# Optimization experiments

Hardware: AMD Instinct MI355X
Metric: run time of the kernel (lower is better)

The kernel has to match this reference:

```python
import jax, jax.numpy as jnp
import numpy as np

EMBED_DIM = 256
SEQ_LEN = 4096
BATCH = 8
ALPHA = 0.99


def setup_inputs() -> dict:
    key = jax.random.key(0)
    k_x, k_w, k_b = jax.random.split(key, 3)
    x = jax.random.normal(k_x, (BATCH, SEQ_LEN, EMBED_DIM), dtype=jnp.float32)
    # nn.Linear(embed_dim, 3*embed_dim): store as [d, 3d] so y = x @ Wqkv + bqkv
    Wqkv = jax.random.normal(k_w, (EMBED_DIM, 3 * EMBED_DIM), dtype=jnp.float32) * (EMBED_DIM ** -0.5)
    bqkv = jax.random.normal(k_b, (3 * EMBED_DIM,), dtype=jnp.float32) * 0.02
    return {"x": x, "Wqkv": Wqkv, "bqkv": bqkv}


def reference(x, Wqkv, bqkv):
    bs, sl, d = x.shape
    qkv = x @ Wqkv + bqkv                      # [bs, sl, 3d]
    q, k, v = jnp.split(qkv, 3, axis=-1)       # each [bs, sl, d]
    # causal * exponential-decay mask: M[i, j] = alpha**(i-j) for j <= i else 0
    i = jnp.arange(sl, dtype=jnp.float32)
    M = jnp.where(i[:, None] >= i[None, :],
                  jnp.power(jnp.float32(ALPHA), i[:, None] - i[None, :]),
                  0.0)                          # [sl, sl]
    scores = jnp.einsum('bqd,bkd->bqk', q, k) / jnp.sqrt(jnp.float32(d))
    out = jnp.einsum('bqk,bkd->bqd', scores * M, v)
    return out
```

## Files before the change

### kernel.cpp

```cpp
#include <hip/hip_runtime.h>

typedef __bf16 bf16x8 __attribute__((ext_vector_type(8)));
typedef float f32x4 __attribute__((ext_vector_type(4)));
typedef unsigned short u16;
typedef unsigned int u32;
typedef u16 u16x4 __attribute__((ext_vector_type(4)));
typedef u16 u16x8 __attribute__((ext_vector_type(8)));

#define L2ALPHA (-0.014499569f)
#define WIN 1024

static __device__ __forceinline__ u16 f2bf(float f) {
    u32 u = __builtin_bit_cast(u32, f);
    return (u16)((u + 0x7FFFu + ((u >> 16) & 1u)) >> 16);
}

static __device__ __forceinline__ void gl2lds16(const void* g, void* l) {
    __builtin_amdgcn_global_load_lds(
        (const __attribute__((address_space(1))) u32*)g,
        (__attribute__((address_space(3))) u32*)l, 16, 0, 0);
}

__global__ __launch_bounds__(256, 2) void proj_kernel(
        const float* __restrict__ x, const float* __restrict__ Wq,
        const float* __restrict__ bias,
        u16* __restrict__ qb, u16* __restrict__ kb, u16* __restrict__ vb)
{
    __shared__ __align__(16) u16 Bs[32 * 128 * 8];
    __shared__ __align__(16) u16 As[4][32 * 40];

    const int tid = threadIdx.x, lane = tid & 63, w = tid >> 6;
    const int l = blockIdx.x;
    const int nb = l % 6;
    const int mt = l / 6;
    const int m0 = mt * 128, n0 = nb * 128;
    const int m = lane & 15, quad = lane >> 4;

    {
        const int col = tid & 127;
        const int khalf = tid >> 7;
        #pragma unroll
        for (int s = 0; s < 32; ++s) {
            int k0 = (khalf + 2 * s) * 4;
            u16x4 h;
            #pragma unroll
            for (int i = 0; i < 4; ++i)
                h[i] = f2bf(Wq[(k0 + i) * 768 + n0 + col]);
            *(u16x4*)&Bs[((k0 >> 3) * 128 + col) * 8 + (k0 & 7)] = h;
        }
    }
    __syncthreads();

    const int r = lane & 31, h = lane >> 5;
    const float* xrow = x + (size_t)(m0 + w * 32 + r) * 256 + h * 16;
    u16* As_w = &As[w][0];

    f32x4 acc[2][8];
    #pragma unroll
    for (int rt = 0; rt < 2; ++rt)
        #pragma unroll
        for (int ct = 0; ct < 8; ++ct)
            acc[rt][ct] = f32x4{0.f, 0.f, 0.f, 0.f};

    float4 g0 = *(const float4*)(xrow + 0);
    float4 g1 = *(const float4*)(xrow + 4);
    float4 g2 = *(const float4*)(xrow + 8);
    float4 g3 = *(const float4*)(xrow + 12);

    for (int kt = 0; kt < 8; ++kt) {
        u16x8 ha, hb;
        ha[0]=f2bf(g0.x); ha[1]=f2bf(g0.y); ha[2]=f2bf(g0.z); ha[3]=f2bf(g0.w);
        ha[4]=f2bf(g1.x); ha[5]=f2bf(g1.y); ha[6]=f2bf(g1.z); ha[7]=f2bf(g1.w);
        hb[0]=f2bf(g2.x); hb[1]=f2bf(g2.y); hb[2]=f2bf(g2.z); hb[3]=f2bf(g2.w);
        hb[4]=f2bf(g3.x); hb[5]=f2bf(g3.y); hb[6]=f2bf(g3.z); hb[7]=f2bf(g3.w);
        *(u16x8*)&As_w[r * 40 + h * 16]     = ha;
        *(u16x8*)&As_w[r * 40 + h * 16 + 8] = hb;

        if (kt < 7) {
            const float* xn = xrow + (kt + 1) * 32;
            g0 = *(const float4*)(xn + 0);
            g1 = *(const float4*)(xn + 4);
            g2 = *(const float4*)(xn + 8);
            g3 = *(const float4*)(xn + 12);
        }

        asm volatile("s_waitcnt lgkmcnt(0)" ::: "memory");

        bf16x8 af[2], bfr[8];
        #pragma unroll
        for (int rt = 0; rt < 2; ++rt)
            af[rt] = *(const bf16x8*)&As_w[(rt * 16 + m) * 40 + quad * 8];
        #pragma unroll
        for (int ct = 0; ct < 8; ++ct)
            bfr[ct] = *(const bf16x8*)&Bs[((kt * 4 + quad) * 128 + ct * 16 + m) * 8];
        #pragma unroll
        for (int rt = 0; rt < 2; ++rt)
            #pragma unroll
            for (int ct = 0; ct < 8; ++ct)
                acc[rt][ct] = __builtin_amdgcn_mfma_f32_16x16x32_bf16(
                    af[rt], bfr[ct], acc[rt][ct], 0, 0, 0);
    }

    const int b = m0 >> 12;
    const int jbase = (m0 & 4095) + w * 32;
    const int d0 = (nb & 1) * 128;

    if (nb < 2) {
        #pragma unroll
        for (int rt = 0; rt < 2; ++rt)
            #pragma unroll
            for (int ct = 0; ct < 8; ++ct) {
                int coll = ct * 16 + m;
                float bv = bias[d0 + coll];
                #pragma unroll
                for (int rr = 0; rr < 4; ++rr) {
                    int row = m0 + w * 32 + rt * 16 + quad * 4 + rr;
                    qb[(size_t)row * 256 + d0 + coll] = f2bf((acc[rt][ct][rr] + bv) * 0.0625f);
                }
            }
    } else if (nb < 4) {
        #pragma unroll
        for (int rt = 0; rt < 2; ++rt)
            #pragma unroll
            for (int ct = 0; ct < 8; ++ct) {
                int d = d0 + ct * 16 + m;
                float bv = bias[256 + d];
                int k8 = d >> 5, qk = (d >> 3) & 3, e = d & 7;
                #pragma unroll
                for (int rr = 0; rr < 4; ++rr) {
                    int j = jbase + rt * 16 + quad * 4 + rr;
                    int jt = j >> 5, jj = j & 31;
                    kb[((((size_t)(b * 128 + jt) * 2 + (jj & 1)) * 8 + k8) * 64 + qk * 16 + (jj >> 1)) * 8 + e]
                        = f2bf(acc[rt][ct][rr] + bv);
                }
            }
    } else {
        #pragma unroll
        for (int rt = 0; rt < 2; ++rt)
            #pragma unroll
            for (int ct = 0; ct < 8; ++ct) {
                int d = d0 + ct * 16 + m;
                float bv = bias[512 + d];
                int dt = d >> 4, mv = d & 15;
                int j = jbase + rt * 16 + quad * 4;
                int jt = j >> 5, qv = (j >> 3) & 3, e0 = j & 7;
                u16x4 hv;
                #pragma unroll
                for (int rr = 0; rr < 4; ++rr) hv[rr] = f2bf(acc[rt][ct][rr] + bv);
                *(u16x4*)&vb[(((size_t)(b * 128 + jt) * 16 + dt) * 64 + qv * 16 + mv) * 8 + e0] = hv;
            }
    }
}

__global__ __launch_bounds__(512, 2) void attn_kernel(
        const u16* __restrict__ qb, const u16* __restrict__ kb,
        const u16* __restrict__ vb, float* __restrict__ out)
{
    __shared__ __align__(16) u16 RB[4][16384];
    __shared__ __align__(16) u16 Ps[8 * 16 * 40];

    const int tid = threadIdx.x, lane = tid & 63, w = tid >> 6;
    const int l = blockIdx.x;
    const int b = l & 7;
    const int m0 = (l >> 3) * 128;
    const int qrow0 = m0 + w * 16;
    const int m = lane & 15, quad = lane >> 4;
    const size_t rowbase = (size_t)b * 4096;
    const size_t pbase = (size_t)b * 128;

    bf16x8 qf[8];
    #pragma unroll
    for (int k8 = 0; k8 < 8; ++k8)
        qf[k8] = *(const bf16x8*)(qb + (rowbase + qrow0 + m) * 256 + k8 * 32 + quad * 8);
    asm volatile("s_waitcnt vmcnt(0)" ::: "memory");

    float Arow[4];
    #pragma unroll
    for (int rr = 0; rr < 4; ++rr)
        Arow[rr] = __builtin_amdgcn_exp2f((float)(quad * 4 + rr) * L2ALPHA);
    const float Em0 = __builtin_amdgcn_exp2f((float)(-2 * m) * L2ALPHA);
    const float Em1 = __builtin_amdgcn_exp2f((float)(-2 * m - 1) * L2ALPHA);

    f32x4 acc[16];
    #pragma unroll
    for (int dt = 0; dt < 16; ++dt)
        acc[dt] = f32x4{0.f, 0.f, 0.f, 0.f};

    int t0 = (m0 - WIN) >> 5; if (t0 < 0) t0 = 0;
    const int t1 = (m0 >> 5) + 3;
    const int nT = t1 - t0 + 1;

    #define STAGE(ix)                                                       \
        do {                                                                \
            const int buf_ = (ix) & 3;                                      \
            const u16* kp_ = kb + (pbase + t0 + (ix)) * 8192;               \
            const u16* vp_ = vb + (pbase + t0 + (ix)) * 8192;               \
            _Pragma("unroll")                                               \
            for (int s_ = 0; s_ < 2; ++s_) {                                \
                int c_ = tid + 512 * s_;                                    \
                gl2lds16(kp_ + (size_t)c_ * 8, &RB[buf_][c_ * 8]);          \
                gl2lds16(vp_ + (size_t)c_ * 8, &RB[buf_][8192 + c_ * 8]);   \
            }                                                               \
        } while (0)

    STAGE(0); STAGE(1); STAGE(2);

    for (int it = 0; it < nT; ++it) {
        if (it <= nT - 3)      asm volatile("s_waitcnt vmcnt(8)" ::: "memory");
        else if (it == nT - 2) asm volatile("s_waitcnt vmcnt(4)" ::: "memory");
        else                   asm volatile("s_waitcnt vmcnt(0)" ::: "memory");
        __builtin_amdgcn_s_barrier();
        asm volatile("" ::: "memory");

        if (it + 3 < nT) STAGE(it + 3);

        const int t = t0 + it;
        const int j0 = t * 32;
        if (j0 <= qrow0 + 15 && j0 + (WIN + 31) >= qrow0) {
            const u16* Kt = &RB[it & 3][0];
            const u16* Vt = &RB[it & 3][8192];

            const float base = __builtin_amdgcn_exp2f((float)(qrow0 - j0) * L2ALPHA);
            const float C0 = base * Em0, C1 = base * Em1;
            const bool needMask = (j0 + 31 > qrow0);

            f32x4 sA{0.f,0.f,0.f,0.f}, sB{0.f,0.f,0.f,0.f};
            #pragma unroll
            for (int k8 = 0; k8 < 8; ++k8) {
                bf16x8 bf0 = *(const bf16x8*)&Kt[(k8 * 64 + lane) * 8];
                sA = __builtin_amdgcn_mfma_f32_16x16x32_bf16(qf[k8], bf0, sA, 0, 0, 0);
            }
            #pragma unroll
            for (int k8 = 0; k8 < 8; ++k8) {
                bf16x8 bf1 = *(const bf16x8*)&Kt[((8 + k8) * 64 + lane) * 8];
                sB = __builtin_amdgcn_mfma_f32_16x16x32_bf16(qf[k8], bf1, sB, 0, 0, 0);
            }

            if (needMask) {
                #pragma unroll
                for (int rr = 0; rr < 4; ++rr) {
                    int ioff = quad * 4 + rr;
                    int dd0 = (qrow0 - j0) + ioff - 2 * m;
                    float w0 = (dd0 >= 0) ? Arow[rr] * C0 : 0.0f;
                    float w1 = (dd0 >= 1) ? Arow[rr] * C1 : 0.0f;
                    u32 pv = (u32)f2bf(sA[rr] * w0) | ((u32)f2bf(sB[rr] * w1) << 16);
                    *(u32*)&Ps[(w * 16 + ioff) * 40 + 2 * m] = pv;
                }
            } else {
                #pragma unroll
                for (int rr = 0; rr < 4; ++rr) {
                    int ioff = quad * 4 + rr;
                    float w0 = Arow[rr] * C0;
                    float w1 = Arow[rr] * C1;
                    u32 pv = (u32)f2bf(sA[rr] * w0) | ((u32)f2bf(sB[rr] * w1) << 16);
                    *(u32*)&Ps[(w * 16 + ioff) * 40 + 2 * m] = pv;
                }
            }
            asm volatile("s_waitcnt lgkmcnt(0)" ::: "memory");

            bf16x8 pa = *(const bf16x8*)&Ps[(w * 16 + m) * 40 + quad * 8];

            #pragma unroll
            for (int dt = 0; dt < 16; ++dt) {
                bf16x8 vf = *(const bf16x8*)&Vt[(dt * 64 + lane) * 8];
                acc[dt] = __builtin_amdgcn_mfma_f32_16x16x32_bf16(pa, vf, acc[dt], 0, 0, 0);
            }
        }
    }

    #pragma unroll
    for (int dt = 0; dt < 16; ++dt)
        #pragma unroll
        for (int rr = 0; rr < 4; ++rr)
            out[(rowbase + qrow0 + quad * 4 + rr) * 256 + dt * 16 + m] = acc[dt][rr];
}

extern "C" void kernel_launch(void* const* d_in, const int* in_sizes, int n_in,
                              void* d_out, int out_size, void* d_ws, size_t ws_size,
                              hipStream_t stream) {
    (void)in_sizes; (void)n_in; (void)out_size; (void)ws_size;
    const float* x    = (const float*)d_in[0];
    const float* Wq   = (const float*)d_in[1];
    const float* bias = (const float*)d_in[2];
    float* outp = (float*)d_out;

    const size_t per = (size_t)8 * 4096 * 256;
    u16* qb = (u16*)d_ws;
    u16* kb = qb + per;
    u16* vb = kb + per;

    proj_kernel<<<1536, 256, 0, stream>>>(x, Wq, bias, qb, kb, vb);
    attn_kernel<<<256, 512, 0, stream>>>(qb, kb, vb, outp);
}
```

Measured before the change: 176.6 us.

## Give each attention wave 32 query rows to reuse K/V fragments

The attention block shrinks from 8 waves to 4, and each wave now handles two 16-row query groups. Every K and V fragment read from LDS therefore feeds two MFMAs instead of one, halving LDS read traffic per FLOP. The cost is more registers per wave (two accumulator sets, two Q fragment sets), launch bounds dropping to 1 block per SIMD set, and fewer waves to hide latency. Staging loads double per thread, and the vmcnt thresholds are adjusted to match.

```diff
diff --git a/kernel.cpp b/kernel.cpp
--- a/kernel.cpp
+++ b/kernel.cpp
@@ -152,39 +152,45 @@
     }
 }
 
-__global__ __launch_bounds__(512, 2) void attn_kernel(
+__global__ __launch_bounds__(256, 1) void attn_kernel(
         const u16* __restrict__ qb, const u16* __restrict__ kb,
         const u16* __restrict__ vb, float* __restrict__ out)
 {
     __shared__ __align__(16) u16 RB[4][16384];
-    __shared__ __align__(16) u16 Ps[8 * 16 * 40];
+    __shared__ __align__(16) u16 Ps[4 * 32 * 40];
 
     const int tid = threadIdx.x, lane = tid & 63, w = tid >> 6;
     const int l = blockIdx.x;
     const int b = l & 7;
     const int m0 = (l >> 3) * 128;
-    const int qrow0 = m0 + w * 16;
+    const int qrow0 = m0 + w * 32;
     const int m = lane & 15, quad = lane >> 4;
     const size_t rowbase = (size_t)b * 4096;
     const size_t pbase = (size_t)b * 128;
 
-    bf16x8 qf[8];
-    #pragma unroll
-    for (int k8 = 0; k8 < 8; ++k8)
-        qf[k8] = *(const bf16x8*)(qb + (rowbase + qrow0 + m) * 256 + k8 * 32 + quad * 8);
+    bf16x8 qf[2][8];
+    #pragma unroll
+    for (int rg = 0; rg < 2; ++rg)
+        #pragma unroll
+        for (int k8 = 0; k8 < 8; ++k8)
+            qf[rg][k8] = *(const bf16x8*)(qb + (rowbase + qrow0 + rg * 16 + m) * 256 + k8 * 32 + quad * 8);
     asm volatile("s_waitcnt vmcnt(0)" ::: "memory");
 
-    float Arow[4];
-    #pragma unroll
-    for (int rr = 0; rr < 4; ++rr)
-        Arow[rr] = __builtin_amdgcn_exp2f((float)(quad * 4 + rr) * L2ALPHA);
+    float Arow[2][4];
+    #pragma unroll
+    for (int rg = 0; rg < 2; ++rg)
+        #pragma unroll
+        for (int rr = 0; rr < 4; ++rr)
+            Arow[rg][rr] = __builtin_amdgcn_exp2f((float)(rg * 16 + quad * 4 + rr) * L2ALPHA);
     const float Em0 = __builtin_amdgcn_exp2f((float)(-2 * m) * L2ALPHA);
     const float Em1 = __builtin_amdgcn_exp2f((float)(-2 * m - 1) * L2ALPHA);
 
-    f32x4 acc[16];
-    #pragma unroll
-    for (int dt = 0; dt < 16; ++dt)
-        acc[dt] = f32x4{0.f, 0.f, 0.f, 0.f};
+    f32x4 acc[2][16];
+    #pragma unroll
+    for (int rg = 0; rg < 2; ++rg)
+        #pragma unroll
+        for (int dt = 0; dt < 16; ++dt)
+            acc[rg][dt] = f32x4{0.f, 0.f, 0.f, 0.f};
 
     int t0 = (m0 - WIN) >> 5; if (t0 < 0) t0 = 0;
     const int t1 = (m0 >> 5) + 3;
@@ -196,8 +202,8 @@
             const u16* kp_ = kb + (pbase + t0 + (ix)) * 8192;               \
             const u16* vp_ = vb + (pbase + t0 + (ix)) * 8192;               \
             _Pragma("unroll")                                               \
-            for (int s_ = 0; s_ < 2; ++s_) {                                \
-                int c_ = tid + 512 * s_;                                    \
+            for (int s_ = 0; s_ < 4; ++s_) {                                \
+                int c_ = tid + 256 * s_;                       \
                 gl2lds16(kp_ + (size_t)c_ * 8, &RB[buf_][c_ * 8]);          \
                 gl2lds16(vp_ + (size_t)c_ * 8, &RB[buf_][8192 + c_ * 8]);   \
             }                                                               \
@@ -206,8 +212,8 @@
     STAGE(0); STAGE(1); STAGE(2);
 
     for (int it = 0; it < nT; ++it) {
-        if (it <= nT - 3)      asm volatile("s_waitcnt vmcnt(8)" ::: "memory");
-        else if (it == nT - 2) asm volatile("s_waitcnt vmcnt(4)" ::: "memory");
+        if (it <= nT - 3)      asm volatile("s_waitcnt vmcnt(16)" ::: "memory");
+        else if (it == nT - 2) asm volatile("s_waitcnt vmcnt(8)" ::: "memory");
         else                   asm volatile("s_waitcnt vmcnt(0)" ::: "memory");
         __builtin_amdgcn_s_barrier();
         asm volatile("" ::: "memory");
@@ -216,63 +222,80 @@
 
         const int t = t0 + it;
         const int j0 = t * 32;
-        if (j0 <= qrow0 + 15 && j0 + (WIN + 31) >= qrow0) {
+        if (j0 <= qrow0 + 31 && j0 + (WIN + 31) >= qrow0) {
             const u16* Kt = &RB[it & 3][0];
             const u16* Vt = &RB[it & 3][8192];
 
             const float base = __builtin_amdgcn_exp2f((float)(qrow0 - j0) * L2ALPHA);
             const float C0 = base * Em0, C1 = base * Em1;
-            const bool needMask = (j0 + 31 > qrow0);
-
-            f32x4 sA{0.f,0.f,0.f,0.f}, sB{0.f,0.f,0.f,0.f};
+            const bool diag = (j0 == qrow0);
+
+            f32x4 sA0{0.f,0.f,0.f,0.f}, sA1{0.f,0.f,0.f,0.f};
+            f32x4 sB0{0.f,0.f,0.f,0.f}, sB1{0.f,0.f,0.f,0.f};
             #pragma unroll
             for (int k8 = 0; k8 < 8; ++k8) {
                 bf16x8 bf0 = *(const bf16x8*)&Kt[(k8 * 64 + lane) * 8];
-                sA = __builtin_amdgcn_mfma_f32_16x16x32_bf16(qf[k8], bf0, sA, 0, 0, 0);
+                sA0 = __builtin_amdgcn_mfma_f32_16x16x32_bf16(qf[0][k8], bf0, sA0, 0, 0, 0);
+                sA1 = __builtin_amdgcn_mfma_f32_16x16x32_bf16(qf[1][k8], bf0, sA1, 0, 0, 0);
             }
             #pragma unroll
             for (int k8 = 0; k8 < 8; ++k8) {
                 bf16x8 bf1 = *(const bf16x8*)&Kt[((8 + k8) * 64 + lane) * 8];
-                sB = __builtin_amdgcn_mfma_f32_16x16x32_bf16(qf[k8], bf1, sB, 0, 0, 0);
-            }
-
-            if (needMask) {
-                #pragma unroll
-                for (int rr = 0; rr < 4; ++rr) {
-                    int ioff = quad * 4 + rr;
-                    int dd0 = (qrow0 - j0) + ioff - 2 * m;
-                    float w0 = (dd0 >= 0) ? Arow[rr] * C0 : 0.0f;
-                    float w1 = (dd0 >= 1) ? Arow[rr] * C1 : 0.0f;
-                    u32 pv = (u32)f2bf(sA[rr] * w0) | ((u32)f2bf(sB[rr] * w1) << 16);
-                    *(u32*)&Ps[(w * 16 + ioff) * 40 + 2 * m] = pv;
+                sB0 = __builtin_amdgcn_mfma_f32_16x16x32_bf16(qf[0][k8], bf1, sB0, 0, 0, 0);
+                sB1 = __builtin_amdgcn_mfma_f32_16x16x32_bf16(qf[1][k8], bf1, sB1, 0, 0, 0);
+            }
+
+            if (diag) {
+                #pragma unroll
+                for (int rg = 0; rg < 2; ++rg) {
+                    f32x4 sh0 = rg ? sA1 : sA0;
+                    f32x4 sh1 = rg ? sB1 : sB0;
+                    #pragma unroll
+                    for (int rr = 0; rr < 4; ++rr) {
+                        int ioff = rg * 16 + quad * 4 + rr;
+                        int dd0 = ioff - 2 * m;
+                        float w0 = (dd0 >= 0) ? Arow[rg][rr] * C0 : 0.0f;
+                        float w1 = (dd0 >= 1) ? Arow[rg][rr] * C1 : 0.0f;
+                        u32 pv = (u32)f2bf(sh0[rr] * w0) | ((u32)f2bf(sh1[rr] * w1) << 16);
+                        *(u32*)&Ps[(w * 32 + ioff) * 40 + 2 * m] = pv;
+                    }
                 }
             } else {
                 #pragma unroll
-                for (int rr = 0; rr < 4; ++rr) {
-                    int ioff = quad * 4 + rr;
-                    float w0 = Arow[rr] * C0;
-                    float w1 = Arow[rr] * C1;
-                    u32 pv = (u32)f2bf(sA[rr] * w0) | ((u32)f2bf(sB[rr] * w1) << 16);
-                    *(u32*)&Ps[(w * 16 + ioff) * 40 + 2 * m] = pv;
+                for (int rg = 0; rg < 2; ++rg) {
+                    f32x4 sh0 = rg ? sA1 : sA0;
+                    f32x4 sh1 = rg ? sB1 : sB0;
+                    #pragma unroll
+                    for (int rr = 0; rr < 4; ++rr) {
+                        int ioff = rg * 16 + quad * 4 + rr;
+                        float w0 = Arow[rg][rr] * C0;
+                        float w1 = Arow[rg][rr] * C1;
+                        u32 pv = (u32)f2bf(sh0[rr] * w0) | ((u32)f2bf(sh1[rr] * w1) << 16);
+                        *(u32*)&Ps[(w * 32 + ioff) * 40 + 2 * m] = pv;
+                    }
                 }
             }
             asm volatile("s_waitcnt lgkmcnt(0)" ::: "memory");
 
-            bf16x8 pa = *(const bf16x8*)&Ps[(w * 16 + m) * 40 + quad * 8];
+            bf16x8 pa0 = *(const bf16x8*)&Ps[(w * 32 + m) * 40 + quad * 8];
+            bf16x8 pa1 = *(const bf16x8*)&Ps[(w * 32 + 16 + m) * 40 + quad * 8];
 
             #pragma unroll
             for (int dt = 0; dt < 16; ++dt) {
                 bf16x8 vf = *(const bf16x8*)&Vt[(dt * 64 + lane) * 8];
-                acc[dt] = __builtin_amdgcn_mfma_f32_16x16x32_bf16(pa, vf, acc[dt], 0, 0, 0);
+                acc[0][dt] = __builtin_amdgcn_mfma_f32_16x16x32_bf16(pa0, vf, acc[0][dt], 0, 0, 0);
+                acc[1][dt] = __builtin_amdgcn_mfma_f32_16x16x32_bf16(pa1, vf, acc[1][dt], 0, 0, 0);
             }
         }
     }
 
     #pragma unroll
-    for (int dt = 0; dt < 16; ++dt)
-        #pragma unroll
-        for (int rr = 0; rr < 4; ++rr)
-            out[(rowbase + qrow0 + quad * 4 + rr) * 256 + dt * 16 + m] = acc[dt][rr];
+    for (int rg = 0; rg < 2; ++rg)
+        #pragma unroll
+        for (int dt = 0; dt < 16; ++dt)
+            #pragma unroll
+            for (int rr = 0; rr < 4; ++rr)
+                out[(rowbase + qrow0 + rg * 16 + quad * 4 + rr) * 256 + dt * 16 + m] = acc[rg][dt][rr];
 }
 
 extern "C" void kernel_launch(void* const* d_in, const int* in_sizes, int n_in,
@@ -290,5 +313,5 @@
     u16* vb = kb + per;
 
     proj_kernel<<<1536, 256, 0, stream>>>(x, Wq, bias, qb, kb, vb);
-    attn_kernel<<<256, 512, 0, stream>>>(qb, kb, vb, outp);
-}
+    attn_kernel<<<256, 256, 0, stream>>>(qb, kb, vb, outp);
+}
```

Result: slower. 193.1 us (+9.4%).
